# Kernel optimization log

Measured on AMD Instinct MI355X. Metric: run time of the kernel, lower is better.

Reference implementation:

```python
import jax, jax.numpy as jnp
import numpy as np

N, D_IN, D_OUT = 4096, 1024, 1024

def setup_inputs() -> dict:
    key = jax.random.key(0)
    k1, k2, k3, k4 = jax.random.split(key, 4)
    x = jax.random.normal(k1, (N, D_IN), dtype=jnp.float32)
    # original uses torch.rand (uniform [0,1)) for params
    w_query = jax.random.uniform(k2, (D_IN, D_OUT), dtype=jnp.float32)
    w_key = jax.random.uniform(k3, (D_IN, D_OUT), dtype=jnp.float32)
    w_value = jax.random.uniform(k4, (D_IN, D_OUT), dtype=jnp.float32)
    return {"x": x, "w_query": w_query, "w_key": w_key, "w_value": w_value}

def reference(x, w_query, w_key, w_value):
    queries = x @ w_query          # [N, d_out]
    keys = x @ w_key               # [N, d_out]
    values = x @ w_value           # [N, d_out]
    scale = keys.shape[-1] ** 0.5
    scores = queries @ keys.T      # [N, N]
    attn = jax.nn.softmax(scores / scale, axis=-1)
    return attn @ values           # [N, d_out]
```

## Files before the change

kernel.cpp:

```cpp
#include <hip/hip_runtime.h>
#include <math.h>

#define NROWS 4096
#define DDIM  1024

typedef __attribute__((ext_vector_type(8))) short short8;
typedef __attribute__((ext_vector_type(4))) float f32x4;

__device__ __forceinline__ ushort f2bf(float v) {
  union { float f; uint32_t u; } c; c.f = v;
  uint32_t u = c.u;
  uint32_t lsb = (u >> 16) & 1u;
  u += 0x7fffu + lsb;
  return (ushort)(u >> 16);
}
__device__ __forceinline__ float bf2f(ushort h) {
  union { uint32_t u; float f; } c; c.u = ((uint32_t)h) << 16;
  return c.f;
}

__device__ __forceinline__ void gll16(const void* g, void* l) {
  __builtin_amdgcn_global_load_lds((const __attribute__((address_space(1))) void*)g,
                                   (__attribute__((address_space(3))) void*)l, 16, 0, 0);
}

__device__ __forceinline__ size_t pidx(int r, int c, int ldt) {
  return ((size_t)((r >> 4) * ldt + (c >> 5))) * 512 +
         ((c >> 3) & 3) * 128 + (r & 15) * 8 + (c & 7);
}
__device__ __forceinline__ size_t pidxs(int r, int c, int ldt) {
  return ((size_t)((r >> 4) * ldt + (c >> 5))) * 1024 +
         ((c >> 3) & 3) * 128 + (r & 15) * 8 + (c & 7);
}

__global__ __launch_bounds__(256) void prep(const float* __restrict__ x,
                                            const float* __restrict__ wq,
                                            const float* __restrict__ wk,
                                            const float* __restrict__ wv,
                                            ushort* Xc,
                                            ushort* Wqc, ushort* Wkc, ushort* Wvh) {
  __shared__ char smem[8448];
  const int b = blockIdx.x, t = threadIdx.x;
  if (b < 512) {
    ushort* xb = (ushort*)smem;
    const int w = t >> 6, l = t & 63;
    ushort* wb = xb + w * 1024;
#pragma unroll 1
    for (int it = 0; it < 4; ++it) {
      int tile = b * 16 + it * 4 + w;
      int tr = tile >> 5, tc = tile & 31;
      const float* src = x + (size_t)(tr * 16) * DDIM + tc * 32;
      int r = l >> 3, cq = l & 7;
#pragma unroll
      for (int hh = 0; hh < 2; ++hh) {
        int rr = r + 8 * hh;
        f32x4 v = __builtin_nontemporal_load(
            (const f32x4*)(src + (size_t)rr * DDIM) + cq);
        int c = cq * 4;
        int intra = ((c >> 3) & 3) * 128 + rr * 8 + (c & 7);
        ushort4 hi, lo;
        hi.x = f2bf(v.x); lo.x = f2bf(v.x - bf2f(hi.x));
        hi.y = f2bf(v.y); lo.y = f2bf(v.y - bf2f(hi.y));
        hi.z = f2bf(v.z); lo.z = f2bf(v.z - bf2f(hi.z));
        hi.w = f2bf(v.w); lo.w = f2bf(v.w - bf2f(hi.w));
        *(ushort4*)(wb + intra) = hi;
        *(ushort4*)(wb + 512 + intra) = lo;
      }
      __syncthreads();
      ushort* dst = Xc + (size_t)tile * 1024;
#pragma unroll
      for (int rd = 0; rd < 2; ++rd)
        *(short8*)(dst + rd * 512 + l * 8) = *(const short8*)(wb + rd * 512 + l * 8);
      __syncthreads();
    }
  } else {
    float (*tl)[33] = (float(*)[33])smem;
    ushort* stg = (ushort*)(smem + 4224);
    const int z = (b - 512) >> 10;
    const int tile = (b - 512) & 1023;
    const float* src = z == 0 ? wq : (z == 1 ? wk : wv);
    const int r0 = (tile >> 5) * 32;
    const int c0 = (tile & 31) * 32;
    const int tx = t & 31, ty = t >> 5;
    for (int i = ty; i < 32; i += 8)
      tl[i][tx] = __builtin_nontemporal_load(&src[(size_t)(r0 + i) * DDIM + c0 + tx]);
    __syncthreads();
    const size_t T0 = (size_t)(c0 >> 4) * 32 + (r0 >> 5);
    if (z == 2) {
      for (int i = ty; i < 32; i += 8) {
        int intra = ((tx >> 3) & 3) * 128 + (i & 15) * 8 + (tx & 7);
        stg[(i >> 4) * 512 + intra] = f2bf(tl[tx][i]);
      }
      __syncthreads();
      int s = t >> 7, idx = (t & 127) * 4;
      *(ushort4*)(Wvh + (T0 + (size_t)s * 32) * 512 + idx) = *(const ushort4*)(stg + s * 512 + idx);
    } else {
      ushort* D = z == 0 ? Wqc : Wkc;
      for (int i = ty; i < 32; i += 8) {
        float v = tl[tx][i];
        ushort h = f2bf(v);
        int intra = ((tx >> 3) & 3) * 128 + (i & 15) * 8 + (tx & 7);
        stg[(i >> 4) * 1024 + intra] = h;
        stg[(i >> 4) * 1024 + 512 + intra] = f2bf(v - bf2f(h));
      }
      __syncthreads();
      int s = t >> 7, idx = (t & 127) * 8;
      *(ushort4*)(D + (T0 + (size_t)s * 32) * 1024 + idx) = *(const ushort4*)(stg + s * 1024 + idx);
      *(ushort4*)(D + (T0 + (size_t)s * 32) * 1024 + idx + 4) = *(const ushort4*)(stg + s * 1024 + idx + 4);
    }
  }
}

__global__ __launch_bounds__(256) void gemm_qkv(const ushort* __restrict__ Xc,
                                                const ushort* __restrict__ Wqc,
                                                const ushort* __restrict__ Wkc,
                                                const ushort* __restrict__ Wvh,
                                                ushort* Qc, ushort* Kc, ushort* Vt) {
  __shared__ char smem[2][32768];
  const int bid = blockIdx.x;
  const int which = bid < 256 ? 2 : (bid < 512 ? 0 : 1);
  const int local = bid & 255;
  const int xcd = local & 7, idx = local >> 3;
  const int t = threadIdx.x;
  const int w = t >> 6, ln = t & 63;
  const int wr = w >> 1, wc = w & 1;
  const int quad = ln >> 4, l16 = ln & 15;

  f32x4 acc[4][4];
#pragma unroll
  for (int i = 0; i < 4; ++i)
#pragma unroll
    for (int j = 0; j < 4; ++j) acc[i][j] = (f32x4){0.f, 0.f, 0.f, 0.f};

  if (which < 2) {
    const int m0 = (xcd * 4 + (idx >> 3)) * 128;
    const int n0 = (idx & 7) * 128;
    const ushort* Bc = which ? Wkc : Wqc;
    const char* srcBase = (w < 2)
        ? (const char*)Xc + (size_t)((m0 >> 4) + (w & 1) * 4) * 65536
        : (const char*)Bc + (size_t)((n0 >> 4) + (w & 1) * 4) * 65536;
    srcBase += ln * 16;
    char* ldsBase = (char*)smem + (w < 2 ? 0 : 16384) + (w & 1) * 8192 + ln * 16;

#pragma unroll
    for (int u = 0; u < 8; ++u)
      gll16(srcBase + (u >> 1) * 65536 + (u & 1) * 1024, ldsBase + u * 1024);
    asm volatile("s_waitcnt vmcnt(0)" ::: "memory");
    __builtin_amdgcn_s_barrier();

    const char* aB = (char*)smem + wr * 8192 + ln * 16;
    const char* bB = (char*)smem + 16384 + wc * 8192 + ln * 16;

#pragma unroll 1
    for (int kt = 0; kt < 32; ++kt) {
      const int cb = (kt & 1) << 15;
      const int nb = ((kt + 1) & 1) << 15;
      if (kt < 31) {
        const char* srcK = srcBase + (size_t)(kt + 1) * 2048;
#pragma unroll
        for (int u = 0; u < 8; ++u)
          gll16(srcK + (u >> 1) * 65536 + (u & 1) * 1024, ldsBase + nb + u * 1024);
      }

      short8 bh[4], bl[4];
#pragma unroll
      for (int j = 0; j < 4; ++j) {
        bh[j] = *(const short8*)(bB + cb + j * 2048);
        bl[j] = *(const short8*)(bB + cb + j * 2048 + 1024);
      }
      __builtin_amdgcn_s_setprio(1);
#pragma unroll
      for (int i = 0; i < 4; ++i) {
        short8 ah = *(const short8*)(aB + cb + i * 2048);
        short8 al = *(const short8*)(aB + cb + i * 2048 + 1024);
#pragma unroll
        for (int j = 0; j < 4; ++j) {
          acc[i][j] = __builtin_amdgcn_mfma_f32_16x16x32_bf16(ah, bh[j], acc[i][j], 0, 0, 0);
          acc[i][j] = __builtin_amdgcn_mfma_f32_16x16x32_bf16(ah, bl[j], acc[i][j], 0, 0, 0);
          acc[i][j] = __builtin_amdgcn_mfma_f32_16x16x32_bf16(al, bh[j], acc[i][j], 0, 0, 0);
        }
      }
      __builtin_amdgcn_s_setprio(0);

      asm volatile("s_waitcnt vmcnt(0)" ::: "memory");
      __builtin_amdgcn_s_barrier();
    }

    const float scale = which ? 1.0f : 0.03125f;
    ushort* D = which ? Kc : Qc;
#pragma unroll
    for (int i = 0; i < 4; ++i)
#pragma unroll
      for (int j = 0; j < 4; ++j) {
        int col = n0 + wc * 64 + j * 16 + l16;
        int rw = m0 + wr * 64 + i * 16 + quad * 4;
#pragma unroll
        for (int r2 = 0; r2 < 4; ++r2) {
          float v = acc[i][j][r2] * scale;
          ushort h = f2bf(v);
          size_t o = pidxs(rw + r2, col, DDIM / 32);
          D[o] = h;
          D[o + 512] = f2bf(v - bf2f(h));
        }
      }
  } else {
    const int m0 = (idx & 7) * 128;
    const int n0 = (xcd * 4 + (idx >> 3)) * 128;
    const char* srcBase = (w < 2)
        ? (const char*)Wvh + (size_t)((m0 >> 4) + (w & 1) * 4) * 32768
        : (const char*)Xc + (size_t)((n0 >> 4) + (w & 1) * 4) * 65536;
    srcBase += ln * 16;
    char* ldsBase = (char*)smem + (w < 2 ? 0 : 8192) + (w & 1) * 4096 + ln * 16;
    const size_t srcStep = (w < 2) ? 1024 : 2048;
    const size_t rowStr = (w < 2) ? 32768 : 65536;

#pragma unroll
    for (int u = 0; u < 4; ++u)
      gll16(srcBase + (size_t)u * rowStr, ldsBase + u * 1024);
    asm volatile("s_waitcnt vmcnt(0)" ::: "memory");
    __builtin_amdgcn_s_barrier();

    const char* aB = (char*)smem + wr * 4096 + ln * 16;
    const char* bB = (char*)smem + 8192 + wc * 4096 + ln * 16;

#pragma unroll 1
    for (int kt = 0; kt < 32; ++kt) {
      const int cb = (kt & 1) << 15;
      const int nb = ((kt + 1) & 1) << 15;
      if (kt < 31) {
        const char* srcK = srcBase + (size_t)(kt + 1) * srcStep;
#pragma unroll
        for (int u = 0; u < 4; ++u)
          gll16(srcK + (size_t)u * rowStr, ldsBase + nb + u * 1024);
      }

      short8 bh[4];
#pragma unroll
      for (int j = 0; j < 4; ++j)
        bh[j] = *(const short8*)(bB + cb + j * 1024);
      __builtin_amdgcn_s_setprio(1);
#pragma unroll
      for (int i = 0; i < 4; ++i) {
        short8 ah = *(const short8*)(aB + cb + i * 1024);
#pragma unroll
        for (int j = 0; j < 4; ++j)
          acc[i][j] = __builtin_amdgcn_mfma_f32_16x16x32_bf16(ah, bh[j], acc[i][j], 0, 0, 0);
      }
      __builtin_amdgcn_s_setprio(0);

      asm volatile("s_waitcnt vmcnt(0)" ::: "memory");
      __builtin_amdgcn_s_barrier();
    }

#pragma unroll
    for (int i = 0; i < 4; ++i)
#pragma unroll
      for (int j = 0; j < 4; ++j) {
        int kv = n0 + wc * 64 + j * 16 + l16;
        int d = m0 + wr * 64 + i * 16 + quad * 4;
#pragma unroll
        for (int r2 = 0; r2 < 4; ++r2)
          Vt[pidx(d + r2, kv, NROWS / 32)] = f2bf(acc[i][j][r2]);
      }
  }
}

__global__ __launch_bounds__(512) void gemm_s(const ushort* __restrict__ Qc,
                                              const ushort* __restrict__ Kc,
                                              float* __restrict__ S) {
  __shared__ char smem[2][65536];
  const int bid = blockIdx.y * 16 + blockIdx.x;
  const int xcd = bid & 7, local = bid >> 3;
  const int m0 = ((xcd >> 1) * 4 + (local & 3)) * 256;
  const int n0 = ((xcd & 1) * 8 + (local >> 2)) * 256;
  const int t = threadIdx.x;
  const int w = t >> 6, ln = t & 63;
  const int wr = w >> 2, wc = w & 3;
  const int quad = ln >> 4, l16 = ln & 15;

  const char* srcBase = (w < 4)
      ? (const char*)Qc + (size_t)((m0 >> 4) + w * 4) * 65536
      : (const char*)Kc + (size_t)((n0 >> 4) + (w - 4) * 4) * 65536;
  srcBase += ln * 16;
  char* ldsBase = (char*)smem + w * 8192 + ln * 16;

  f32x4 acc[8][4];
#pragma unroll
  for (int i = 0; i < 8; ++i)
#pragma unroll
    for (int j = 0; j < 4; ++j) acc[i][j] = (f32x4){0.f, 0.f, 0.f, 0.f};

#pragma unroll
  for (int u = 0; u < 8; ++u)
    gll16(srcBase + (u >> 1) * 65536 + (u & 1) * 1024, ldsBase + u * 1024);
  asm volatile("s_waitcnt vmcnt(0)" ::: "memory");
  __builtin_amdgcn_s_barrier();

  const char* aB = (char*)smem + (wr * 8) * 2048 + ln * 16;
  const char* bB = (char*)smem + 32768 + (wc * 4) * 2048 + ln * 16;

#pragma unroll 1
  for (int kt = 0; kt < 32; ++kt) {
    const int cb = (kt & 1) << 16;
    const int nb = ((kt + 1) & 1) << 16;
    const char* srcK = srcBase + (size_t)(kt + 1) * 2048;

    if (kt < 31) {
#pragma unroll
      for (int u = 0; u < 8; ++u)
        gll16(srcK + (u >> 1) * 65536 + (u & 1) * 1024, ldsBase + nb + u * 1024);
    }

    short8 bh[4], bl[4];
#pragma unroll
    for (int j = 0; j < 4; ++j) {
      bh[j] = *(const short8*)(bB + cb + j * 2048);
      bl[j] = *(const short8*)(bB + cb + j * 2048 + 1024);
    }

#pragma unroll
    for (int p = 0; p < 4; ++p) {
      short8 ah0 = *(const short8*)(aB + cb + (2 * p) * 2048);
      short8 al0 = *(const short8*)(aB + cb + (2 * p) * 2048 + 1024);
      short8 ah1 = *(const short8*)(aB + cb + (2 * p + 1) * 2048);
      short8 al1 = *(const short8*)(aB + cb + (2 * p + 1) * 2048 + 1024);
      __builtin_amdgcn_s_setprio(1);
#pragma unroll
      for (int j_ = 0; j_ < 4; ++j_) {
        acc[2 * p][j_] = __builtin_amdgcn_mfma_f32_16x16x32_bf16(ah0, bh[j_], acc[2 * p][j_], 0, 0, 0);
        acc[2 * p][j_] = __builtin_amdgcn_mfma_f32_16x16x32_bf16(ah0, bl[j_], acc[2 * p][j_], 0, 0, 0);
        acc[2 * p][j_] = __builtin_amdgcn_mfma_f32_16x16x32_bf16(al0, bh[j_], acc[2 * p][j_], 0, 0, 0);
        acc[2 * p + 1][j_] = __builtin_amdgcn_mfma_f32_16x16x32_bf16(ah1, bh[j_], acc[2 * p + 1][j_], 0, 0, 0);
        acc[2 * p + 1][j_] = __builtin_amdgcn_mfma_f32_16x16x32_bf16(ah1, bl[j_], acc[2 * p + 1][j_], 0, 0, 0);
        acc[2 * p + 1][j_] = __builtin_amdgcn_mfma_f32_16x16x32_bf16(al1, bh[j_], acc[2 * p + 1][j_], 0, 0, 0);
      }
      __builtin_amdgcn_s_setprio(0);
    }

    asm volatile("s_waitcnt vmcnt(0)" ::: "memory");
    __builtin_amdgcn_s_barrier();
  }

#pragma unroll
  for (int i = 0; i < 8; ++i)
#pragma unroll
    for (int j = 0; j < 4; ++j) {
      int col = n0 + wc * 64 + j * 16 + l16;
      int rw = m0 + wr * 128 + i * 16 + quad * 4;
#pragma unroll
      for (int r2 = 0; r2 < 4; ++r2)
        S[(size_t)(rw + r2) * NROWS + col] = acc[i][j][r2];
    }
}

__global__ __launch_bounds__(256) void softmax_pack(const float* __restrict__ S,
                                                    ushort* __restrict__ P) {
  const int row = blockIdx.x, t = threadIdx.x;
  const float* Sr = S + (size_t)row * NROWS;
  const f32x4* S4 = (const f32x4*)Sr;
  f32x4 v[4];
  float mx = -3.4e38f;
#pragma unroll
  for (int c = 0; c < 4; ++c) {
    v[c] = S4[c * 256 + t];
    mx = fmaxf(mx, fmaxf(fmaxf(v[c].x, v[c].y), fmaxf(v[c].z, v[c].w)));
  }
  __shared__ float red[4];
  for (int o = 32; o >= 1; o >>= 1) mx = fmaxf(mx, __shfl_xor(mx, o));
  int wv = t >> 6, ln = t & 63;
  if (ln == 0) red[wv] = mx;
  __syncthreads();
  mx = fmaxf(fmaxf(red[0], red[1]), fmaxf(red[2], red[3]));
  float s = 0.f;
#pragma unroll
  for (int c = 0; c < 4; ++c) {
    v[c].x = __expf(v[c].x - mx);
    v[c].y = __expf(v[c].y - mx);
    v[c].z = __expf(v[c].z - mx);
    v[c].w = __expf(v[c].w - mx);
    s += v[c].x + v[c].y + v[c].z + v[c].w;
  }
  for (int o = 32; o >= 1; o >>= 1) s += __shfl_xor(s, o);
  __syncthreads();
  if (ln == 0) red[wv] = s;
  __syncthreads();
  s = red[0] + red[1] + red[2] + red[3];
  float inv = 1.f / s;
#pragma unroll
  for (int c = 0; c < 4; ++c) {
    ushort4 h;
    h.x = f2bf(v[c].x * inv);
    h.y = f2bf(v[c].y * inv);
    h.z = f2bf(v[c].z * inv);
    h.w = f2bf(v[c].w * inv);
    int kt = 32 * c + (t >> 3);
    *(ushort4*)(P + (size_t)kt * 131072 + (size_t)row * 32 + 4 * (t & 7)) = h;
  }
}

__global__ __launch_bounds__(256) void gemm_pv(const ushort* __restrict__ P,
                                               const ushort* __restrict__ Vt,
                                               float* __restrict__ Out) {
  const int n0 = blockIdx.x * 128, m0 = blockIdx.y * 128;
  const int t = threadIdx.x;
  const int wv = t >> 6, ln = t & 63;
  const int quad = ln >> 4, l16 = ln & 15;
  const int arb = (wv >> 1) * 64, crb = (wv & 1) * 64;
  const int ra = (m0 + arb) >> 4;
  const int rb = (n0 + crb) >> 4;

  f32x4 acc[4][4];
#pragma unroll
  for (int i = 0; i < 4; ++i)
#pragma unroll
    for (int j = 0; j < 4; ++j) acc[i][j] = (f32x4){0.f, 0.f, 0.f, 0.f};

  uint oA[4], oB[4];
#pragma unroll
  for (int i = 0; i < 4; ++i)
    oA[i] = (uint)(ra + i) * 512u + (uint)(ln & 15) * 32u + (uint)(ln >> 4) * 8u;
#pragma unroll
  for (int j = 0; j < 4; ++j)
    oB[j] = (uint)(rb + j) * 65536u + (uint)ln * 8u;

  short8 a0[4], b0[4], a1[4], b1[4];

#define PV_LOAD(sidx, AH, BH)                                                \
  {                                                                          \
    uint ka_ = (uint)(sidx)*131072u;                                         \
    uint kb_ = (uint)(sidx)*512u;                                            \
    _Pragma("unroll") for (int i_ = 0; i_ < 4; ++i_)                         \
      AH[i_] = *(const short8*)(P + oA[i_] + ka_);                           \
    _Pragma("unroll") for (int j_ = 0; j_ < 4; ++j_)                         \
      BH[j_] = *(const short8*)(Vt + oB[j_] + kb_);                          \
  }

#define PV_MFMA(AH, BH)                                                      \
  {                                                                          \
    __builtin_amdgcn_s_setprio(1);                                           \
    _Pragma("unroll") for (int j_ = 0; j_ < 4; ++j_)                         \
      _Pragma("unroll") for (int i_ = 0; i_ < 4; ++i_)                       \
        acc[i_][j_] = __builtin_amdgcn_mfma_f32_16x16x32_bf16(               \
            AH[i_], BH[j_], acc[i_][j_], 0, 0, 0);                           \
    __builtin_amdgcn_s_setprio(0);                                           \
  }

  PV_LOAD(0, a0, b0);
#pragma unroll 1
  for (int s = 0; s < 126; s += 2) {
    PV_LOAD(s + 1, a1, b1);
    PV_MFMA(a0, b0);
    PV_LOAD(s + 2, a0, b0);
    PV_MFMA(a1, b1);
  }
  PV_LOAD(127, a1, b1);
  PV_MFMA(a0, b0);
  PV_MFMA(a1, b1);
#undef PV_LOAD
#undef PV_MFMA

#pragma unroll
  for (int i = 0; i < 4; ++i)
#pragma unroll
    for (int j = 0; j < 4; ++j) {
      int col = n0 + crb + j * 16 + l16;
      int rw = m0 + arb + i * 16 + quad * 4;
#pragma unroll
      for (int r2 = 0; r2 < 4; ++r2)
        Out[(size_t)(rw + r2) * DDIM + col] = acc[i][j][r2];
    }
}

extern "C" void kernel_launch(void* const* d_in, const int* in_sizes, int n_in,
                              void* d_out, int out_size, void* d_ws, size_t ws_size,
                              hipStream_t stream) {
  const float* x  = (const float*)d_in[0];
  const float* wq = (const float*)d_in[1];
  const float* wk = (const float*)d_in[2];
  const float* wv = (const float*)d_in[3];
  char* ws = (char*)d_ws;
  const size_t MB = 1u << 20;

  ushort* Vt  = (ushort*)(ws + 0);
  ushort* Qc  = (ushort*)(ws + 8 * MB);
  ushort* Kc  = (ushort*)(ws + 24 * MB);
  ushort* Pp  = (ushort*)(ws + 8 * MB);
  ushort* Xc  = (ushort*)(ws + 40 * MB);
  ushort* Wqc = (ushort*)(ws + 56 * MB);
  ushort* Wkc = (ushort*)(ws + 60 * MB);
  ushort* Wvh = (ushort*)(ws + 64 * MB);
  float*  S   = (float*)(ws + 40 * MB);
  float*  Out = (float*)d_out;

  prep<<<3584, 256, 0, stream>>>(x, wq, wk, wv, Xc, Wqc, Wkc, Wvh);
  gemm_qkv<<<768, 256, 0, stream>>>(Xc, Wqc, Wkc, Wvh, Qc, Kc, Vt);
  gemm_s<<<dim3(16, 16), 512, 0, stream>>>(Qc, Kc, S);
  softmax_pack<<<NROWS, 256, 0, stream>>>(S, Pp);
  gemm_pv<<<dim3(8, 32), 256, 0, stream>>>(Pp, Vt, Out);
}
```

Measured before the change: 284.1 us.

## Replace double-buffered LDS DMA with register-staged single-buffer prefetch in gemm_s

The S-GEMM kernel stops using direct global-to-LDS loads into two 64KB buffers. It now prefetches the next K tile into registers, computes on a single 64KB LDS buffer, then writes the registers to LDS between two barriers. Launch bounds are raised to a minimum of 4 blocks per CU to push occupancy. The change halves LDS use but adds 32 VGPRs per thread for staging plus an extra barrier per iteration, and the launch-bounds constraint may force register spills given the 128-register accumulator.

```diff
diff --git a/kernel.cpp b/kernel.cpp
--- a/kernel.cpp
+++ b/kernel.cpp
@@ -265,10 +265,10 @@
   }
 }
 
-__global__ __launch_bounds__(512) void gemm_s(const ushort* __restrict__ Qc,
-                                              const ushort* __restrict__ Kc,
-                                              float* __restrict__ S) {
-  __shared__ char smem[2][65536];
+__global__ __launch_bounds__(512, 4) void gemm_s(const ushort* __restrict__ Qc,
+                                                 const ushort* __restrict__ Kc,
+                                                 float* __restrict__ S) {
+  __shared__ char smem[65536];
   const int bid = blockIdx.y * 16 + blockIdx.x;
   const int xcd = bid & 7, local = bid >> 3;
   const int m0 = ((xcd >> 1) * 4 + (local & 3)) * 256;
@@ -282,7 +282,7 @@
       ? (const char*)Qc + (size_t)((m0 >> 4) + w * 4) * 65536
       : (const char*)Kc + (size_t)((n0 >> 4) + (w - 4) * 4) * 65536;
   srcBase += ln * 16;
-  char* ldsBase = (char*)smem + w * 8192 + ln * 16;
+  char* ldsW = (char*)smem + w * 8192 + ln * 16;
 
   f32x4 acc[8][4];
 #pragma unroll
@@ -292,7 +292,7 @@
 
 #pragma unroll
   for (int u = 0; u < 8; ++u)
-    gll16(srcBase + (u >> 1) * 65536 + (u & 1) * 1024, ldsBase + u * 1024);
+    gll16(srcBase + (u >> 1) * 65536 + (u & 1) * 1024, ldsW + u * 1024);
   asm volatile("s_waitcnt vmcnt(0)" ::: "memory");
   __builtin_amdgcn_s_barrier();
 
@@ -301,29 +301,27 @@
 
 #pragma unroll 1
   for (int kt = 0; kt < 32; ++kt) {
-    const int cb = (kt & 1) << 16;
-    const int nb = ((kt + 1) & 1) << 16;
-    const char* srcK = srcBase + (size_t)(kt + 1) * 2048;
-
+    short8 g[8];
     if (kt < 31) {
+      const char* srcK = srcBase + (size_t)(kt + 1) * 2048;
 #pragma unroll
       for (int u = 0; u < 8; ++u)
-        gll16(srcK + (u >> 1) * 65536 + (u & 1) * 1024, ldsBase + nb + u * 1024);
+        g[u] = *(const short8*)(srcK + (u >> 1) * 65536 + (u & 1) * 1024);
     }
 
     short8 bh[4], bl[4];
 #pragma unroll
     for (int j = 0; j < 4; ++j) {
-      bh[j] = *(const short8*)(bB + cb + j * 2048);
-      bl[j] = *(const short8*)(bB + cb + j * 2048 + 1024);
+      bh[j] = *(const short8*)(bB + j * 2048);
+      bl[j] = *(const short8*)(bB + j * 2048 + 1024);
     }
 
 #pragma unroll
     for (int p = 0; p < 4; ++p) {
-      short8 ah0 = *(const short8*)(aB + cb + (2 * p) * 2048);
-      short8 al0 = *(const short8*)(aB + cb + (2 * p) * 2048 + 1024);
-      short8 ah1 = *(const short8*)(aB + cb + (2 * p + 1) * 2048);
-      short8 al1 = *(const short8*)(aB + cb + (2 * p + 1) * 2048 + 1024);
+      short8 ah0 = *(const short8*)(aB + (2 * p) * 2048);
+      short8 al0 = *(const short8*)(aB + (2 * p) * 2048 + 1024);
+      short8 ah1 = *(const short8*)(aB + (2 * p + 1) * 2048);
+      short8 al1 = *(const short8*)(aB + (2 * p + 1) * 2048 + 1024);
       __builtin_amdgcn_s_setprio(1);
 #pragma unroll
       for (int j_ = 0; j_ < 4; ++j_) {
@@ -337,8 +335,15 @@
       __builtin_amdgcn_s_setprio(0);
     }
 
-    asm volatile("s_waitcnt vmcnt(0)" ::: "memory");
-    __builtin_amdgcn_s_barrier();
+    if (kt < 31) {
+      __builtin_amdgcn_s_barrier();
+      asm volatile("s_waitcnt vmcnt(0)" ::: "memory");
+#pragma unroll
+      for (int u = 0; u < 8; ++u)
+        *(short8*)(ldsW + u * 1024) = g[u];
+      asm volatile("s_waitcnt lgkmcnt(0)" ::: "memory");
+      __builtin_amdgcn_s_barrier();
+    }
   }
 
 #pragma unroll
```

Measured after the change: 667.4 us. 2.35x slower.
